# Kernel optimization log

Measured on AMD Instinct MI355X. Metric: run time of the kernel, lower is better.

The kernel has to match this reference:

```python
import jax, jax.numpy as jnp
import numpy as np

MAX_SET_SIZE = 8


def setup_inputs() -> dict:
    key = jax.random.key(0)
    ks = jax.random.split(key, 8)
    n_items, L, d_v = 8192, 64, 128
    n_chains, hidden = 32768, 128
    v = jax.random.normal(ks[0], (n_items, L, d_v), dtype=jnp.float32)
    batch_idx = jax.random.randint(ks[1], (n_chains,), 0, n_items, dtype=jnp.int32)
    mask = jax.random.randint(ks[2], (n_chains, L), 0, 2) > 0
    count = jax.random.randint(ks[3], (n_chains,), 0, 64, dtype=jnp.int32)
    in_dim = MAX_SET_SIZE * d_v + 1
    W1 = jax.random.normal(ks[4], (in_dim, hidden), dtype=jnp.float32) / np.sqrt(in_dim)
    b1 = jnp.zeros((hidden,), dtype=jnp.float32)
    W2 = jax.random.normal(ks[5], (hidden, d_v), dtype=jnp.float32) / np.sqrt(hidden)
    b2 = jnp.zeros((d_v,), dtype=jnp.float32)
    return {"v": v, "batch_idx": batch_idx, "mask": mask, "count": count,
            "W1": W1, "b1": b1, "W2": W2, "b2": b2}


def reference(v, batch_idx, mask, count, W1, b1, W2, b2):
    n_chains, L = mask.shape
    d_v = v.shape[-1]
    K = MAX_SET_SIZE  # k_keep = min(max_set_size, L) = 8 since L >= 8
    # score = mask * (L - pos): earlier positions score higher; top_k picks
    # the first K masked positions (ties impossible among masked entries).
    pos = jnp.arange(L, dtype=jnp.float32)
    scores = mask.astype(jnp.float32) * (jnp.float32(L) - pos)[None, :]
    top_scores, top_idx = jax.lax.top_k(scores, K)        # [n_chains, K]
    picked = top_scores > 0
    sortable = jnp.where(picked, top_idx, L)              # sentinel L for unpicked
    order = jnp.argsort(sortable, axis=1)                 # restore index order
    sortable = jnp.take_along_axis(sortable, order, axis=1)
    picked = jnp.take_along_axis(picked, order, axis=1)
    safe_idx = jnp.where(picked, sortable, 0)
    # Fused gather: v[batch_idx[c], safe_idx[c, k], :] -> [n_chains, K, d_v]
    packed = v[batch_idx[:, None], safe_idx]
    packed = packed * picked[..., None].astype(v.dtype)
    flat = packed.reshape(n_chains, K * d_v)
    log_count = jnp.log1p(count.astype(v.dtype))[:, None]
    x = jnp.concatenate([flat, log_count], axis=-1)       # [n_chains, K*d_v + 1]
    h = jax.nn.gelu(x @ W1 + b1, approximate=False)       # exact GELU (torch default)
    return h @ W2 + b2
```

## Files before the change

kernel.cpp:

```cpp
#include <hip/hip_runtime.h>
#include <hip/hip_bf16.h>
#include <math.h>


typedef __attribute__((ext_vector_type(8))) short bf16x8;
typedef __attribute__((ext_vector_type(4))) float f32x4;

#define NCHAINS 32768
#define LPOS    64
#define DV      128
#define HID     128
#define KDIM    1024
#define CPB     32

__device__ __forceinline__ unsigned short cvt_bf16(float a) {
  unsigned u = __float_as_uint(a);
  u += 0x7fffu + ((u >> 16) & 1u);
  return (unsigned short)(u >> 16);
}
__device__ __forceinline__ unsigned pk2_bf16(float a, float b) {
  unsigned ua = __float_as_uint(a), ub = __float_as_uint(b);
  ua += 0x7fffu + ((ua >> 16) & 1u);
  ub += 0x7fffu + ((ub >> 16) & 1u);
  return (ua >> 16) | (ub & 0xffff0000u);
}
__device__ __forceinline__ float gelu_exact(float x) {
  return 0.5f * x * (1.0f + erff(x * 0.70710678118654752f));
}

__global__ __launch_bounds__(256) void prep_kernel(
    const float* __restrict__ W1, const float* __restrict__ W2,
    unsigned short* __restrict__ W1t, unsigned short* __restrict__ W2t,
    float* __restrict__ zr) {
  int id = blockIdx.x * 256 + threadIdx.x;
  if (id < HID * KDIM) {
    int n = id >> 10, k = id & 1023;
    W1t[id] = cvt_bf16(W1[k * HID + n]);
  }
  if (id < HID * HID) {
    int n = id >> 7, k = id & 127;
    W2t[id] = cvt_bf16(W2[k * HID + n]);
  }
  if (id < DV) zr[id] = 0.0f;
}

__global__ __launch_bounds__(256, 2) void agg_mlp_kernel(
    const float* __restrict__ v, const int* __restrict__ batch_idx,
    const int* __restrict__ mask, const int* __restrict__ count,
    const float* __restrict__ W1, const float* __restrict__ b1,
    const float* __restrict__ W2, const float* __restrict__ b2,
    const unsigned short* __restrict__ W1t, const unsigned short* __restrict__ W2t,
    const float* __restrict__ zr, float* __restrict__ out) {
  __shared__ const float* s_ptr[CPB][8];
  __shared__ float s_logc[CPB];
  __shared__ unsigned short s_X[CPB][KDIM + 8];
  __shared__ unsigned short s_H[CPB][HID + 8];

  const int tid = threadIdx.x;
  const int blk = blockIdx.x;

  if (tid < CPB) {
    int c = blk * CPB + tid;
    const int4* mp = (const int4*)(mask + (size_t)c * LPOS);
    unsigned long long m64 = 0;
    #pragma unroll
    for (int q = 0; q < 16; q++) {
      int4 mm = mp[q];
      unsigned long long b = (mm.x != 0 ? 1ull : 0ull) | (mm.y != 0 ? 2ull : 0ull) |
                             (mm.z != 0 ? 4ull : 0ull) | (mm.w != 0 ? 8ull : 0ull);
      m64 |= b << (q * 4);
    }
    const float* base = v + (size_t)batch_idx[c] * (LPOS * DV);
    #pragma unroll
    for (int s = 0; s < 8; s++) {
      const float* p;
      if (m64) {
        int pos = __ffsll(m64) - 1;
        m64 &= (m64 - 1);
        p = base + pos * DV;
      } else {
        p = zr;
      }
      s_ptr[tid][s] = p;
    }
    s_logc[tid] = log1pf((float)count[c]);
  }
  __syncthreads();

  {
    const int chain = tid >> 3, l8 = tid & 7;
    #pragma unroll
    for (int s = 0; s < 8; s++) {
      const float4* p = (const float4*)s_ptr[chain][s];
      #pragma unroll
      for (int part = 0; part < 4; part++) {
        int f4 = part * 8 + l8;
        float4 vv = p[f4];
        unsigned lo = pk2_bf16(vv.x, vv.y);
        unsigned hi = pk2_bf16(vv.z, vv.w);
        *(uint2*)&s_X[chain][s * DV + f4 * 4] = make_uint2(lo, hi);
      }
    }
  }
  __syncthreads();

  const int l = tid & 63, w = tid >> 6;
  const int m = l & 15, kq = l >> 4;
  const int n0 = (2 * w) * 16 + m;
  const int n1 = n0 + 16;

  f32x4 acc00 = {0.f, 0.f, 0.f, 0.f}, acc01 = {0.f, 0.f, 0.f, 0.f};
  f32x4 acc10 = {0.f, 0.f, 0.f, 0.f}, acc11 = {0.f, 0.f, 0.f, 0.f};

  const unsigned short* bb0 = W1t + (size_t)n0 * KDIM + kq * 8;
  const unsigned short* bb1 = W1t + (size_t)n1 * KDIM + kq * 8;

  #pragma unroll 4
  for (int ch = 0; ch < 32; ch++) {
    int k0 = ch * 32 + kq * 8;
    bf16x8 a0 = *(const bf16x8*)&s_X[m][k0];
    bf16x8 a1 = *(const bf16x8*)&s_X[m + 16][k0];
    bf16x8 bf0 = *(const bf16x8*)(bb0 + ch * 32);
    bf16x8 bf1 = *(const bf16x8*)(bb1 + ch * 32);
    acc00 = __builtin_amdgcn_mfma_f32_16x16x32_bf16(a0, bf0, acc00, 0, 0, 0);
    acc01 = __builtin_amdgcn_mfma_f32_16x16x32_bf16(a0, bf1, acc01, 0, 0, 0);
    acc10 = __builtin_amdgcn_mfma_f32_16x16x32_bf16(a1, bf0, acc10, 0, 0, 0);
    acc11 = __builtin_amdgcn_mfma_f32_16x16x32_bf16(a1, bf1, acc11, 0, 0, 0);
  }

  {
    float w1l0 = W1[KDIM * HID + n0];
    float w1l1 = W1[KDIM * HID + n1];
    float b10 = b1[n0], b11 = b1[n1];
    #pragma unroll
    for (int r = 0; r < 4; r++) {
      int row = kq * 4 + r;
      float lc0 = s_logc[row], lc1 = s_logc[16 + row];
      float h;
      h = acc00[r] + lc0 * w1l0 + b10; s_H[row][n0]      = cvt_bf16(gelu_exact(h));
      h = acc01[r] + lc0 * w1l1 + b11; s_H[row][n1]      = cvt_bf16(gelu_exact(h));
      h = acc10[r] + lc1 * w1l0 + b10; s_H[16 + row][n0] = cvt_bf16(gelu_exact(h));
      h = acc11[r] + lc1 * w1l1 + b11; s_H[16 + row][n1] = cvt_bf16(gelu_exact(h));
    }
  }
  __syncthreads();

  f32x4 d00 = {0.f, 0.f, 0.f, 0.f}, d01 = {0.f, 0.f, 0.f, 0.f};
  f32x4 d10 = {0.f, 0.f, 0.f, 0.f}, d11 = {0.f, 0.f, 0.f, 0.f};
  const unsigned short* cb0 = W2t + n0 * HID + kq * 8;
  const unsigned short* cb1 = W2t + n1 * HID + kq * 8;

  #pragma unroll
  for (int ch = 0; ch < 4; ch++) {
    int k0 = ch * 32 + kq * 8;
    bf16x8 a0 = *(const bf16x8*)&s_H[m][k0];
    bf16x8 a1 = *(const bf16x8*)&s_H[m + 16][k0];
    bf16x8 bf0 = *(const bf16x8*)(cb0 + ch * 32);
    bf16x8 bf1 = *(const bf16x8*)(cb1 + ch * 32);
    d00 = __builtin_amdgcn_mfma_f32_16x16x32_bf16(a0, bf0, d00, 0, 0, 0);
    d01 = __builtin_amdgcn_mfma_f32_16x16x32_bf16(a0, bf1, d01, 0, 0, 0);
    d10 = __builtin_amdgcn_mfma_f32_16x16x32_bf16(a1, bf0, d10, 0, 0, 0);
    d11 = __builtin_amdgcn_mfma_f32_16x16x32_bf16(a1, bf1, d11, 0, 0, 0);
  }

  {
    float b20 = b2[n0], b21 = b2[n1];
    #pragma unroll
    for (int r = 0; r < 4; r++) {
      int row = kq * 4 + r;
      size_t c0 = (size_t)(blk * CPB + row) * DV;
      size_t c1 = (size_t)(blk * CPB + 16 + row) * DV;
      out[c0 + n0] = d00[r] + b20;
      out[c0 + n1] = d01[r] + b21;
      out[c1 + n0] = d10[r] + b20;
      out[c1 + n1] = d11[r] + b21;
    }
  }
}

extern "C" void kernel_launch(void* const* d_in, const int* in_sizes, int n_in,
                              void* d_out, int out_size, void* d_ws, size_t ws_size,
                              hipStream_t stream) {
  const float* v          = (const float*)d_in[0];
  const int* batch_idx    = (const int*)d_in[1];
  const int* mk           = (const int*)d_in[2];
  const int* count        = (const int*)d_in[3];
  const float* W1         = (const float*)d_in[4];
  const float* b1         = (const float*)d_in[5];
  const float* W2         = (const float*)d_in[6];
  const float* b2         = (const float*)d_in[7];
  float* out              = (float*)d_out;

  char* ws = (char*)d_ws;
  unsigned short* W1t = (unsigned short*)ws;
  unsigned short* W2t = (unsigned short*)(ws + 262144);
  float* zr           = (float*)(ws + 262144 + 32768);

  prep_kernel<<<512, 256, 0, stream>>>(W1, W2, W1t, W2t, zr);
  agg_mlp_kernel<<<NCHAINS / CPB, 256, 0, stream>>>(
      v, batch_idx, mk, count, W1, b1, W2, b2, W1t, W2t, zr, out);
}
```

Measured before the change: 394.9 us.

## Load gathered rows directly into MFMA fragments and pre-pack weights in fragment order

Removes the shared-memory staging of the gathered input matrix. Each lane now reads its fp32 slice of the gathered v rows straight from global memory and converts it to bf16 in registers as the MFMA A operand. The weights are repacked in the prep kernel into MFMA fragment order, so each B load is one contiguous 16-byte access per lane. Dropping the large shared buffer lets the occupancy hint rise from 2 to 4 blocks per CU. In exchange, every wave loads the A rows it needs from global memory itself, so rows are fetched redundantly across waves with no shared-memory reuse.

```diff
diff --git a/kernel.cpp b/kernel.cpp
--- a/kernel.cpp
+++ b/kernel.cpp
@@ -24,36 +24,46 @@
   ub += 0x7fffu + ((ub >> 16) & 1u);
   return (ua >> 16) | (ub & 0xffff0000u);
 }
+__device__ __forceinline__ bf16x8 pack8(float4 a, float4 b) {
+  union { bf16x8 v; unsigned u[4]; } r;
+  r.u[0] = pk2_bf16(a.x, a.y);
+  r.u[1] = pk2_bf16(a.z, a.w);
+  r.u[2] = pk2_bf16(b.x, b.y);
+  r.u[3] = pk2_bf16(b.z, b.w);
+  return r.v;
+}
 __device__ __forceinline__ float gelu_exact(float x) {
   return 0.5f * x * (1.0f + erff(x * 0.70710678118654752f));
 }
 
 __global__ __launch_bounds__(256) void prep_kernel(
     const float* __restrict__ W1, const float* __restrict__ W2,
-    unsigned short* __restrict__ W1t, unsigned short* __restrict__ W2t,
+    unsigned short* __restrict__ W1p, unsigned short* __restrict__ W2p,
     float* __restrict__ zr) {
   int id = blockIdx.x * 256 + threadIdx.x;
-  if (id < HID * KDIM) {
-    int n = id >> 10, k = id & 1023;
-    W1t[id] = cvt_bf16(W1[k * HID + n]);
-  }
-  if (id < HID * HID) {
-    int n = id >> 7, k = id & 127;
-    W2t[id] = cvt_bf16(W2[k * HID + n]);
+  {
+    int j = id & 7, lx = (id >> 3) & 63, nt = (id >> 9) & 7, ch = id >> 12;
+    int k = ch * 32 + ((lx >> 4) & 3) * 8 + j;
+    int n = nt * 16 + (lx & 15);
+    W1p[id] = cvt_bf16(W1[k * HID + n]);
+    if (id < 16384) {
+      int ch2 = id >> 12;
+      int k2 = ch2 * 32 + ((lx >> 4) & 3) * 8 + j;
+      W2p[id] = cvt_bf16(W2[k2 * HID + n]);
+    }
   }
   if (id < DV) zr[id] = 0.0f;
 }
 
-__global__ __launch_bounds__(256, 2) void agg_mlp_kernel(
+__global__ __launch_bounds__(256, 4) void agg_mlp_kernel(
     const float* __restrict__ v, const int* __restrict__ batch_idx,
     const int* __restrict__ mask, const int* __restrict__ count,
     const float* __restrict__ W1, const float* __restrict__ b1,
-    const float* __restrict__ W2, const float* __restrict__ b2,
-    const unsigned short* __restrict__ W1t, const unsigned short* __restrict__ W2t,
+    const float* __restrict__ b2,
+    const unsigned short* __restrict__ W1p, const unsigned short* __restrict__ W2p,
     const float* __restrict__ zr, float* __restrict__ out) {
   __shared__ const float* s_ptr[CPB][8];
   __shared__ float s_logc[CPB];
-  __shared__ unsigned short s_X[CPB][KDIM + 8];
   __shared__ unsigned short s_H[CPB][HID + 8];
 
   const int tid = threadIdx.x;
@@ -87,45 +97,34 @@
   }
   __syncthreads();
 
-  {
-    const int chain = tid >> 3, l8 = tid & 7;
-    #pragma unroll
-    for (int s = 0; s < 8; s++) {
-      const float4* p = (const float4*)s_ptr[chain][s];
-      #pragma unroll
-      for (int part = 0; part < 4; part++) {
-        int f4 = part * 8 + l8;
-        float4 vv = p[f4];
-        unsigned lo = pk2_bf16(vv.x, vv.y);
-        unsigned hi = pk2_bf16(vv.z, vv.w);
-        *(uint2*)&s_X[chain][s * DV + f4 * 4] = make_uint2(lo, hi);
-      }
-    }
-  }
-  __syncthreads();
-
   const int l = tid & 63, w = tid >> 6;
   const int m = l & 15, kq = l >> 4;
-  const int n0 = (2 * w) * 16 + m;
-  const int n1 = n0 + 16;
+  const int nt0 = 2 * w, nt1 = 2 * w + 1;
+  const int n0 = nt0 * 16 + m, n1 = n0 + 16;
 
   f32x4 acc00 = {0.f, 0.f, 0.f, 0.f}, acc01 = {0.f, 0.f, 0.f, 0.f};
   f32x4 acc10 = {0.f, 0.f, 0.f, 0.f}, acc11 = {0.f, 0.f, 0.f, 0.f};
 
-  const unsigned short* bb0 = W1t + (size_t)n0 * KDIM + kq * 8;
-  const unsigned short* bb1 = W1t + (size_t)n1 * KDIM + kq * 8;
-
-  #pragma unroll 4
-  for (int ch = 0; ch < 32; ch++) {
-    int k0 = ch * 32 + kq * 8;
-    bf16x8 a0 = *(const bf16x8*)&s_X[m][k0];
-    bf16x8 a1 = *(const bf16x8*)&s_X[m + 16][k0];
-    bf16x8 bf0 = *(const bf16x8*)(bb0 + ch * 32);
-    bf16x8 bf1 = *(const bf16x8*)(bb1 + ch * 32);
-    acc00 = __builtin_amdgcn_mfma_f32_16x16x32_bf16(a0, bf0, acc00, 0, 0, 0);
-    acc01 = __builtin_amdgcn_mfma_f32_16x16x32_bf16(a0, bf1, acc01, 0, 0, 0);
-    acc10 = __builtin_amdgcn_mfma_f32_16x16x32_bf16(a1, bf0, acc10, 0, 0, 0);
-    acc11 = __builtin_amdgcn_mfma_f32_16x16x32_bf16(a1, bf1, acc11, 0, 0, 0);
+  for (int s = 0; s < 8; s++) {
+    const float* pa0 = s_ptr[m][s] + kq * 8;
+    const float* pa1 = s_ptr[m + 16][s] + kq * 8;
+    #pragma unroll
+    for (int q = 0; q < 4; q++) {
+      const int off = q * 32;
+      float4 x0 = *(const float4*)(pa0 + off);
+      float4 x1 = *(const float4*)(pa0 + off + 4);
+      float4 y0 = *(const float4*)(pa1 + off);
+      float4 y1 = *(const float4*)(pa1 + off + 4);
+      const int ch = s * 4 + q;
+      bf16x8 b0 = *(const bf16x8*)(W1p + (size_t)((ch * 8 + nt0) * 64 + l) * 8);
+      bf16x8 b1 = *(const bf16x8*)(W1p + (size_t)((ch * 8 + nt1) * 64 + l) * 8);
+      bf16x8 a0 = pack8(x0, x1);
+      bf16x8 a1 = pack8(y0, y1);
+      acc00 = __builtin_amdgcn_mfma_f32_16x16x32_bf16(a0, b0, acc00, 0, 0, 0);
+      acc01 = __builtin_amdgcn_mfma_f32_16x16x32_bf16(a0, b1, acc01, 0, 0, 0);
+      acc10 = __builtin_amdgcn_mfma_f32_16x16x32_bf16(a1, b0, acc10, 0, 0, 0);
+      acc11 = __builtin_amdgcn_mfma_f32_16x16x32_bf16(a1, b1, acc11, 0, 0, 0);
+    }
   }
 
   {
@@ -147,20 +146,18 @@
 
   f32x4 d00 = {0.f, 0.f, 0.f, 0.f}, d01 = {0.f, 0.f, 0.f, 0.f};
   f32x4 d10 = {0.f, 0.f, 0.f, 0.f}, d11 = {0.f, 0.f, 0.f, 0.f};
-  const unsigned short* cb0 = W2t + n0 * HID + kq * 8;
-  const unsigned short* cb1 = W2t + n1 * HID + kq * 8;
 
   #pragma unroll
   for (int ch = 0; ch < 4; ch++) {
     int k0 = ch * 32 + kq * 8;
     bf16x8 a0 = *(const bf16x8*)&s_H[m][k0];
     bf16x8 a1 = *(const bf16x8*)&s_H[m + 16][k0];
-    bf16x8 bf0 = *(const bf16x8*)(cb0 + ch * 32);
-    bf16x8 bf1 = *(const bf16x8*)(cb1 + ch * 32);
-    d00 = __builtin_amdgcn_mfma_f32_16x16x32_bf16(a0, bf0, d00, 0, 0, 0);
-    d01 = __builtin_amdgcn_mfma_f32_16x16x32_bf16(a0, bf1, d01, 0, 0, 0);
-    d10 = __builtin_amdgcn_mfma_f32_16x16x32_bf16(a1, bf0, d10, 0, 0, 0);
-    d11 = __builtin_amdgcn_mfma_f32_16x16x32_bf16(a1, bf1, d11, 0, 0, 0);
+    bf16x8 b0 = *(const bf16x8*)(W2p + (size_t)((ch * 8 + nt0) * 64 + l) * 8);
+    bf16x8 b1 = *(const bf16x8*)(W2p + (size_t)((ch * 8 + nt1) * 64 + l) * 8);
+    d00 = __builtin_amdgcn_mfma_f32_16x16x32_bf16(a0, b0, d00, 0, 0, 0);
+    d01 = __builtin_amdgcn_mfma_f32_16x16x32_bf16(a0, b1, d01, 0, 0, 0);
+    d10 = __builtin_amdgcn_mfma_f32_16x16x32_bf16(a1, b0, d10, 0, 0, 0);
+    d11 = __builtin_amdgcn_mfma_f32_16x16x32_bf16(a1, b1, d11, 0, 0, 0);
   }
 
   {
@@ -192,11 +189,11 @@
   float* out              = (float*)d_out;
 
   char* ws = (char*)d_ws;
-  unsigned short* W1t = (unsigned short*)ws;
-  unsigned short* W2t = (unsigned short*)(ws + 262144);
+  unsigned short* W1p = (unsigned short*)ws;
+  unsigned short* W2p = (unsigned short*)(ws + 262144);
   float* zr           = (float*)(ws + 262144 + 32768);
 
-  prep_kernel<<<512, 256, 0, stream>>>(W1, W2, W1t, W2t, zr);
+  prep_kernel<<<512, 256, 0, stream>>>(W1, W2, W1p, W2p, zr);
   agg_mlp_kernel<<<NCHAINS / CPB, 256, 0, stream>>>(
-      v, batch_idx, mk, count, W1, b1, W2, b2, W1t, W2t, zr, out);
+      v, batch_idx, mk, count, W1, b1, b2, W1p, W2p, zr, out);
 }
```

Measured after the change: 390.5 us. About the same (-1.1%).
